# Optimization experiments

Hardware: AMD Instinct MI355X
Metric: run time of the kernel (lower is better)

## Reference

```python
import jax, jax.numpy as jnp
import numpy as np
from jax import lax

B, V, K, E = 32768, 256, 4, 2048
INTERVENTION_STRENGTH = 1.0
PROP_SCALE = 0.1
N_ROUNDS = 3


def setup_inputs() -> dict:
    key = jax.random.key(0)
    ks = jax.random.split(key, 20)
    s = 0.02
    return {
        "original_data": jax.random.normal(ks[0], (B, V), jnp.float32),
        "intervention_values": jax.random.normal(ks[1], (B, K), jnp.float32),
        "strengths": jax.random.uniform(ks[2], (E,), jnp.float32),
        "intervention_variables": jnp.arange(K, dtype=jnp.int32),
        "cause_idx": jax.random.randint(ks[3], (E,), 0, V, jnp.int32),
        "effect_idx": jax.random.randint(ks[4], (E,), 0, V, jnp.int32),
        # per-intervention-variable estimator MLPs: Linear(V,64) -> ReLU -> Linear(64,V)
        "est_W1": jax.random.normal(ks[5], (K, 64, V), jnp.float32) * s,
        "est_b1": jnp.zeros((K, 64), jnp.float32),
        "est_W2": jax.random.normal(ks[6], (K, V, 64), jnp.float32) * s,
        "est_b2": jnp.zeros((K, V), jnp.float32),
        # plausibility scorer: Linear(3V,128) -> ReLU -> Linear(128,64) -> ReLU -> Linear(64,1) -> Sigmoid
        "pl_W1": jax.random.normal(ks[7], (128, 3 * V), jnp.float32) * s,
        "pl_b1": jnp.zeros((128,), jnp.float32),
        "pl_W2": jax.random.normal(ks[8], (64, 128), jnp.float32) * s,
        "pl_b2": jnp.zeros((64,), jnp.float32),
        "pl_W3": jax.random.normal(ks[9], (1, 64), jnp.float32) * s,
        "pl_b3": jnp.zeros((1,), jnp.float32),
    }


def _propagate(data, cause_idx, effect_idx, strengths):
    # Faithful sequential in-place edge updates (effect of edge k may feed edge k+1).
    def step(d, ces):
        c, e, st = ces
        infl = d[:, c] * (st * PROP_SCALE)  # [B]
        return d.at[:, e].add(infl), None

    def round_body(d, _):
        d, _ = lax.scan(step, d, (cause_idx, effect_idx, strengths))
        return d, None

    d, _ = lax.scan(round_body, data, None, length=N_ROUNDS)
    return d


def reference(original_data, intervention_values, strengths,
              est_W1, est_b1, est_W2, est_b2,
              pl_W1, pl_b1, pl_W2, pl_b2, pl_W3, pl_b3,
              intervention_variables, cause_idx, effect_idx):
    x = original_data  # [B, V]
    ivars = intervention_variables  # [K] int, constant

    # do-intervention: overwrite selected columns
    intervened = x.at[:, ivars].set(intervention_values)  # [B, V]

    # intervention effect estimators, vectorized over the K intervened variables
    h = jax.nn.relu(jnp.einsum('bv,kov->bko', x, est_W1) + est_b1)          # [B, K, 64]
    eff = jnp.einsum('bko,kvo->bkv', h, est_W2) + est_b2                     # [B, K, V]
    mag = jnp.abs(intervention_values - x[:, ivars])                         # [B, K]
    intervention_effects = jnp.einsum('bkv,bk->bv', eff, mag) * INTERVENTION_STRENGTH  # [B, V]

    # sequential causal propagation over edge list, 3 rounds
    final_cf = _propagate(intervened + intervention_effects, cause_idx, effect_idx, strengths)

    # plausibility scorer MLP
    pin = jnp.concatenate([x, intervened, final_cf], axis=1)                 # [B, 3V]
    p = jax.nn.relu(pin @ pl_W1.T + pl_b1)
    p = jax.nn.relu(p @ pl_W2.T + pl_b2)
    plaus = jax.nn.sigmoid(p @ pl_W3.T + pl_b3)                              # [B, 1]

    impact = jnp.linalg.norm(final_cf - x, axis=1, keepdims=True)            # [B, 1]
    return final_cf, intervention_effects, plaus, impact
```

## Files before the change

kernel.cpp:

```cpp
#include <hip/hip_runtime.h>

#define BDIM 32768
#define VDIM 256
#define KVAR 4
#define EDIM 2048
#define SEGS 16
#define SEGLEN 128

typedef __attribute__((ext_vector_type(8))) short short8;
typedef __attribute__((ext_vector_type(4))) float f32x4;

__device__ __forceinline__ unsigned short f2b(float f){
  union { float f; unsigned u; } v; v.f = f;
  unsigned r = v.u + 0x7FFFu + ((v.u >> 16) & 1u);
  return (unsigned short)(r >> 16);
}
__device__ __forceinline__ float b2f(unsigned short h){
  union { unsigned u; float f; } v; v.u = ((unsigned)h) << 16;
  return v.f;
}
__device__ __forceinline__ short8 ldb8(const unsigned short* p){
  return *(const short8*)p;
}

__device__ __forceinline__ void gl_lds16(const unsigned short* g, unsigned short* l){
  __builtin_amdgcn_global_load_lds(
      (const __attribute__((address_space(1))) unsigned int*)g,
      (__attribute__((address_space(3))) unsigned int*)l, 16, 0, 0);
}

__device__ __forceinline__ void stage256(const unsigned short* Bt, int kB,
                                         int w, int lane, unsigned short* Bs){
#pragma unroll
  for (int i = 0; i < 4; i++){
    int g8 = i*8 + w;
    int r  = g8*8 + (lane >> 3);
    int s  = lane & 7;
    gl_lds16(Bt + (size_t)r*VDIM + kB + ((s ^ (r & 7)) << 3),
             Bs + (size_t)g8*512);
  }
}
__device__ __forceinline__ void stage128(const unsigned short* Bt, int kB,
                                         int w, int lane, unsigned short* Bs){
#pragma unroll
  for (int i = 0; i < 2; i++){
    int g8 = i*8 + w;
    int r  = g8*8 + (lane >> 3);
    int s  = lane & 7;
    gl_lds16(Bt + (size_t)r*VDIM + kB + ((s ^ (r & 7)) << 3),
             Bs + (size_t)g8*512);
  }
}

__device__ __forceinline__ short8 bs_frag(const unsigned short* Bs, int c, int klocal){
  int slot = klocal >> 3;
  return *(const short8*)&Bs[(size_t)c*64 + (((slot ^ (c & 7))) << 3)];
}

template<int NF>
__device__ __forceinline__ void mm_rA(const short8 (&a)[2][2], const unsigned short* Bs,
                                      int c0, int kb, f32x4 (&acc)[2][NF])
{
#pragma unroll
  for (int k = 0; k < 2; k++){
#pragma unroll
    for (int fn = 0; fn < NF; fn++){
      int c = c0 + fn*16;
      short8 b = bs_frag(Bs, c, k*32 + kb);
      acc[0][fn] = __builtin_amdgcn_mfma_f32_16x16x32_bf16(a[k][0], b, acc[0][fn], 0, 0, 0);
      acc[1][fn] = __builtin_amdgcn_mfma_f32_16x16x32_bf16(a[k][1], b, acc[1][fn], 0, 0, 0);
    }
  }
}
template<int NF>
__device__ __forceinline__ void mm_lA(const unsigned short* Alds, int ldaE,
                                      const unsigned short* Bs,
                                      int rl0, int c0, int kb, int kB,
                                      f32x4 (&acc)[2][NF])
{
  int sw = (rl0 & 7) << 3;
#pragma unroll
  for (int k = 0; k < 2; k++){
    int ka = kB + k*32 + kb;
    short8 a0 = *(const short8*)&Alds[(size_t)rl0 * ldaE + (ka ^ sw)];
    short8 a1 = *(const short8*)&Alds[(size_t)(rl0+16) * ldaE + (ka ^ sw)];
#pragma unroll
    for (int fn = 0; fn < NF; fn++){
      int c = c0 + fn*16;
      short8 b = bs_frag(Bs, c, k*32 + kb);
      acc[0][fn] = __builtin_amdgcn_mfma_f32_16x16x32_bf16(a0, b, acc[0][fn], 0, 0, 0);
      acc[1][fn] = __builtin_amdgcn_mfma_f32_16x16x32_bf16(a1, b, acc[1][fn], 0, 0, 0);
    }
  }
}
template<int NF, int KSZ>
__device__ __forceinline__ void mm_l1(const unsigned short* Alds, int ldaE,
                                      const unsigned short* Bt, int ldb,
                                      int rl0, int c0, int kb,
                                      f32x4 (&acc)[NF])
{
  int sw = (rl0 & 7) << 3;
#pragma unroll
  for (int k0 = 0; k0 < KSZ; k0 += 32){
    int ka = k0 + kb;
    short8 a0 = *(const short8*)&Alds[(size_t)rl0 * ldaE + (ka ^ sw)];
#pragma unroll
    for (int fn = 0; fn < NF; fn++){
      short8 b = ldb8(Bt + (size_t)(c0 + fn*16)*ldb + ka);
      acc[fn] = __builtin_amdgcn_mfma_f32_16x16x32_bf16(a0, b, acc[fn], 0, 0, 0);
    }
  }
}

__global__ __launch_bounds__(256) void prep_seg(
    const float* X, const float* IV, const int* ivars,
    const float* eW1, const float* eW2, const float* pW1, const float* pW2,
    const int* cidx, const int* eidx, const float* stren,
    unsigned short* XB,
    unsigned short* bt1, unsigned short* bt2,
    unsigned short* w1ab, unsigned short* w1c,
    unsigned short* w2bf, float* w1bcol, int* colmap,
    float* delta, float* segs)
{
  if (blockIdx.x < 1024){
    __shared__ int lc[SEGLEN];
    __shared__ int le[SEGLEN];
    __shared__ float la[SEGLEN];
    int bid = blockIdx.x;
    int seg = bid >> 6;
    int rowbase = (bid & 63) * 4;
    int w = threadIdx.x >> 6, lane = threadIdx.x & 63;
    int row = rowbase + w;
    int k0 = seg * SEGLEN;
    for (int t = threadIdx.x; t < SEGLEN; t += 256){
      lc[t] = cidx[k0 + t]; le[t] = eidx[k0 + t]; la[t] = stren[k0 + t] * 0.1f;
    }
    __syncthreads();
    float r0 = (row == lane)        ? 1.f : 0.f;
    float r1 = (row == lane + 64)   ? 1.f : 0.f;
    float r2 = (row == lane + 128)  ? 1.f : 0.f;
    float r3 = (row == lane + 192)  ? 1.f : 0.f;
    for (int t = 0; t < SEGLEN; t++){
      int cs = __builtin_amdgcn_readfirstlane(lc[t]);
      int es = __builtin_amdgcn_readfirstlane(le[t]);
      float a = la[t];
      float vr;
      switch (cs >> 6){ case 0: vr = r0; break; case 1: vr = r1; break;
                        case 2: vr = r2; break; default: vr = r3; }
      float v = __shfl(vr, cs & 63, 64);
      float add = (lane == (es & 63)) ? a * v : 0.f;
      switch (es >> 6){ case 0: r0 += add; break; case 1: r1 += add; break;
                        case 2: r2 += add; break; default: r3 += add; }
    }
    float* out = segs + (size_t)seg * 65536 + (size_t)row * 256;
    out[lane] = r0; out[lane + 64] = r1; out[lane + 128] = r2; out[lane + 192] = r3;
    return;
  }
  int stride = 1024 * 256;
  int g0 = (blockIdx.x - 1024) * 256 + threadIdx.x;
  for (int i = g0; i < (BDIM * VDIM) / 8; i += stride){
    const float* p = X + (size_t)i * 8;
    f32x4 lo = *(const f32x4*)p;
    f32x4 hi = *(const f32x4*)(p + 4);
    short8 r;
    r[0]=(short)f2b(lo[0]); r[1]=(short)f2b(lo[1]); r[2]=(short)f2b(lo[2]); r[3]=(short)f2b(lo[3]);
    r[4]=(short)f2b(hi[0]); r[5]=(short)f2b(hi[1]); r[6]=(short)f2b(hi[2]); r[7]=(short)f2b(hi[3]);
    *(short8*)(XB + (size_t)i * 8) = r;
  }
  for (int i = g0; i < 65536; i += stride) bt1[i] = f2b(eW1[i]);
  for (int i = g0; i < 65536; i += stride){
    int v = i >> 8, r = i & 255;
    bt2[i] = f2b(eW2[(r >> 6) * 16384 + v * 64 + (r & 63)]);
  }
  for (int i = g0; i < 32768; i += stride){
    int o = i >> 8, v = i & 255;
    w1ab[i] = f2b(pW1[o*768 + v] + pW1[o*768 + 256 + v]);
    w1c[i]  = f2b(pW1[o*768 + 512 + v]);
  }
  for (int i = g0; i < 8192; i += stride) w2bf[i] = f2b(pW2[i]);
  for (int i = g0; i < 512; i += stride){
    int o = i >> 2, k = i & 3;
    w1bcol[i] = pW1[o*768 + 256 + ivars[k]];
  }
  for (int i = g0; i < VDIM; i += stride){
    int m = -1;
#pragma unroll
    for (int k = 0; k < KVAR; k++) if (ivars[k] == i) m = k;
    colmap[i] = m;
  }
  for (int i = g0; i < BDIM * KVAR; i += stride){
    int b = i >> 2, k = i & 3;
    delta[i] = IV[i] - X[(size_t)b * VDIM + ivars[k]];
  }
}

__global__ __launch_bounds__(256) void combine4(const float* S, float* Out)
{
  int m = blockIdx.x >> 6;
  int rb = (blockIdx.x & 63) * 4;
  int c = threadIdx.x;
  __shared__ float v[4][256];
  const float* base = S + (size_t)m * 4 * 65536;
#pragma unroll
  for (int r = 0; r < 4; r++) v[r][c] = base[(size_t)(rb + r) * 256 + c];
  __syncthreads();
  for (int p = 1; p < 4; p++){
    const float* Bm = base + (size_t)p * 65536;
    float a0 = 0.f, a1 = 0.f, a2 = 0.f, a3 = 0.f;
    for (int k = 0; k < 256; k += 4){
      f32x4 v0 = *(const f32x4*)&v[0][k];
      f32x4 v1 = *(const f32x4*)&v[1][k];
      f32x4 v2 = *(const f32x4*)&v[2][k];
      f32x4 v3 = *(const f32x4*)&v[3][k];
#pragma unroll
      for (int j = 0; j < 4; j++){
        float bk = Bm[(size_t)(k + j) * 256 + c];
        a0 += v0[j] * bk; a1 += v1[j] * bk; a2 += v2[j] * bk; a3 += v3[j] * bk;
      }
    }
    __syncthreads();
    v[0][c] = a0; v[1][c] = a1; v[2][c] = a2; v[3][c] = a3;
    __syncthreads();
  }
#pragma unroll
  for (int r = 0; r < 4; r++) Out[(size_t)m * 65536 + (size_t)(rb + r) * 256 + c] = v[r][c];
}

__global__ __launch_bounds__(256) void powM(const float* R, unsigned short* Mt)
{
  int rb = blockIdx.x * 4;
  int c = threadIdx.x;
  __shared__ float v[4][256];
#pragma unroll
  for (int r = 0; r < 4; r++) v[r][c] = R[(size_t)(rb + r) * 256 + c];
  __syncthreads();
  for (int p = 0; p < 2; p++){
    float a0 = 0.f, a1 = 0.f, a2 = 0.f, a3 = 0.f;
    for (int k = 0; k < 256; k += 4){
      f32x4 v0 = *(const f32x4*)&v[0][k];
      f32x4 v1 = *(const f32x4*)&v[1][k];
      f32x4 v2 = *(const f32x4*)&v[2][k];
      f32x4 v3 = *(const f32x4*)&v[3][k];
#pragma unroll
      for (int j = 0; j < 4; j++){
        float bk = R[(size_t)(k + j) * 256 + c];
        a0 += v0[j] * bk; a1 += v1[j] * bk; a2 += v2[j] * bk; a3 += v3[j] * bk;
      }
    }
    __syncthreads();
    v[0][c] = a0; v[1][c] = a1; v[2][c] = a2; v[3][c] = a3;
    __syncthreads();
  }
#pragma unroll
  for (int r = 0; r < 4; r++) Mt[(size_t)c * 256 + (rb + r)] = f2b(v[r][c]);
}

__global__ __launch_bounds__(512, 4) void mega(
    const float* IV, const unsigned short* XB,
    const unsigned short* Bt1, const unsigned short* Bt2, const unsigned short* Mt,
    const unsigned short* W1ab, const unsigned short* W1c, const unsigned short* W2bf,
    const float* eb1, const float* eb2, const float* delta, const int* colmap,
    const float* w1bcol, const float* pb1, const float* pb2,
    const float* W3, const float* pb3,
    float* effOut, float* outF, float* plausOut, float* impOut)
{
  __shared__ unsigned short buf[64 * 256];
  __shared__ unsigned short Bs[256 * 64];
  __shared__ float impLds[64 * 4];
  int tid = threadIdx.x, w = tid >> 6, lane = tid & 63;
  int rowg = w >> 2, colg = w & 3;
  int rowBlk = blockIdx.x * 64;
  int rl0 = rowg * 32 + (lane & 15);
  int r0 = rowBlk + rl0;
  int colBase = colg * 64;
  int c0 = colBase + (lane & 15);
  int kb = (lane >> 4) * 8;
  f32x4 acc[2][4];

#pragma unroll
  for (int fm = 0; fm < 2; fm++)
#pragma unroll
    for (int fn = 0; fn < 4; fn++) acc[fm][fn] = (f32x4){0.f,0.f,0.f,0.f};
  for (int kc = 0; kc < 4; kc++){
    int kB = kc * 64;
    stage256(Bt1, kB, w, lane, Bs);
    short8 a[2][2];
#pragma unroll
    for (int k = 0; k < 2; k++)
#pragma unroll
      for (int m = 0; m < 2; m++)
        a[k][m] = ldb8(XB + (size_t)(r0 + m*16)*VDIM + kB + k*32 + kb);
    __syncthreads();
    __builtin_amdgcn_s_setprio(1);
    mm_rA<4>(a, Bs, c0, kb, acc);
    __builtin_amdgcn_s_setprio(0);
    __syncthreads();
  }
  {
    float b1v[4];
#pragma unroll
    for (int fn = 0; fn < 4; fn++) b1v[fn] = eb1[colBase + fn*16 + (lane & 15)];
#pragma unroll
    for (int fm = 0; fm < 2; fm++)
#pragma unroll
      for (int i = 0; i < 4; i++){
        int rl = rowg*32 + fm*16 + (lane >> 4)*4 + i;
        int gr = rowBlk + rl;
        float mg = fabsf(delta[gr*4 + colg]);
        int sw = (rl & 7) << 3;
#pragma unroll
        for (int fn = 0; fn < 4; fn++){
          int col = colBase + fn*16 + (lane & 15);
          float h = acc[fm][fn][i] + b1v[fn];
          h = h > 0.f ? h : 0.f;
          buf[(size_t)rl*256 + (col ^ sw)] = f2b(h * mg);
        }
      }
  }
  __syncthreads();

#pragma unroll
  for (int fm = 0; fm < 2; fm++)
#pragma unroll
    for (int fn = 0; fn < 4; fn++) acc[fm][fn] = (f32x4){0.f,0.f,0.f,0.f};
  for (int kc = 0; kc < 4; kc++){
    int kB = kc * 64;
    stage256(Bt2, kB, w, lane, Bs);
    __syncthreads();
    __builtin_amdgcn_s_setprio(1);
    mm_lA<4>(buf, 256, Bs, rl0, c0, kb, kB, acc);
    __builtin_amdgcn_s_setprio(0);
    __syncthreads();
  }
  {
    float bb0[4], bb1[4], bb2[4], bb3[4];
    int imv[4];
#pragma unroll
    for (int fn = 0; fn < 4; fn++){
      int col = colBase + fn*16 + (lane & 15);
      bb0[fn] = eb2[col]; bb1[fn] = eb2[256 + col];
      bb2[fn] = eb2[512 + col]; bb3[fn] = eb2[768 + col];
      imv[fn] = colmap[col];
    }
#pragma unroll
    for (int fm = 0; fm < 2; fm++)
#pragma unroll
      for (int i = 0; i < 4; i++){
        int rl = rowg*32 + fm*16 + (lane >> 4)*4 + i;
        int gr = rowBlk + rl;
        f32x4 dl = *(const f32x4*)&delta[gr*4];
        float d0a = fabsf(dl[0]), d1a = fabsf(dl[1]), d2a = fabsf(dl[2]), d3a = fabsf(dl[3]);
        int sw = (rl & 7) << 3;
#pragma unroll
        for (int fn = 0; fn < 4; fn++){
          int col = colBase + fn*16 + (lane & 15);
          float eff = acc[fm][fn][i] + d0a*bb0[fn] + d1a*bb1[fn] + d2a*bb2[fn] + d3a*bb3[fn];
          size_t idx = (size_t)gr*VDIM + col;
          __builtin_nontemporal_store(eff, &effOut[idx]);
          float base = (imv[fn] >= 0) ? IV[gr*4 + imv[fn]] : b2f(XB[idx]);
          buf[(size_t)rl*256 + (col ^ sw)] = f2b(base + eff);
        }
      }
  }
  __syncthreads();

#pragma unroll
  for (int fm = 0; fm < 2; fm++)
#pragma unroll
    for (int fn = 0; fn < 4; fn++) acc[fm][fn] = (f32x4){0.f,0.f,0.f,0.f};
  for (int kc = 0; kc < 4; kc++){
    int kB = kc * 64;
    stage256(Mt, kB, w, lane, Bs);
    __syncthreads();
    __builtin_amdgcn_s_setprio(1);
    mm_lA<4>(buf, 256, Bs, rl0, c0, kb, kB, acc);
    __builtin_amdgcn_s_setprio(0);
    __syncthreads();
  }
  {
#pragma unroll
    for (int fm = 0; fm < 2; fm++)
#pragma unroll
      for (int i = 0; i < 4; i++){
        int rl = rowg*32 + fm*16 + (lane >> 4)*4 + i;
        int gr = rowBlk + rl;
        int sw = (rl & 7) << 3;
        float ss = 0.f;
#pragma unroll
        for (int fn = 0; fn < 4; fn++){
          int col = colBase + fn*16 + (lane & 15);
          size_t idx = (size_t)gr*VDIM + col;
          float fv = acc[fm][fn][i];
          __builtin_nontemporal_store(fv, &outF[idx]);
          buf[(size_t)rl*256 + (col ^ sw)] = f2b(fv);
          float d = fv - b2f(XB[idx]);
          ss += d * d;
        }
        ss += __shfl_xor(ss, 1, 64); ss += __shfl_xor(ss, 2, 64);
        ss += __shfl_xor(ss, 4, 64); ss += __shfl_xor(ss, 8, 64);
        if ((lane & 15) == 0) impLds[rl*4 + colg] = ss;
      }
  }
  __syncthreads();

  {
    f32x4 a4[2][2];
#pragma unroll
    for (int fm = 0; fm < 2; fm++)
#pragma unroll
      for (int fn = 0; fn < 2; fn++) a4[fm][fn] = (f32x4){0.f,0.f,0.f,0.f};
    int c4 = colg * 32 + (lane & 15);
    for (int kc = 0; kc < 4; kc++){
      int kB = kc * 64;
      stage128(W1ab, kB, w, lane, Bs);
      stage128(W1c,  kB, w, lane, Bs + 8192);
      short8 a[2][2];
#pragma unroll
      for (int k = 0; k < 2; k++)
#pragma unroll
        for (int m = 0; m < 2; m++)
          a[k][m] = ldb8(XB + (size_t)(r0 + m*16)*VDIM + kB + k*32 + kb);
      __syncthreads();
      __builtin_amdgcn_s_setprio(1);
      mm_rA<2>(a, Bs, c4, kb, a4);
      mm_lA<2>(buf, 256, Bs + 8192, rl0, c4, kb, kB, a4);
      __builtin_amdgcn_s_setprio(0);
      __syncthreads();
    }
    float bv[2];
    f32x4 wb[2];
#pragma unroll
    for (int fn = 0; fn < 2; fn++){
      int col = colg*32 + fn*16 + (lane & 15);
      bv[fn] = pb1[col];
      wb[fn] = *(const f32x4*)&w1bcol[col*4];
    }
#pragma unroll
    for (int fm = 0; fm < 2; fm++)
#pragma unroll
      for (int i = 0; i < 4; i++){
        int rl = rowg*32 + fm*16 + (lane >> 4)*4 + i;
        int gr = rowBlk + rl;
        f32x4 dl = *(const f32x4*)&delta[gr*4];
        int sw = (rl & 7) << 3;
#pragma unroll
        for (int fn = 0; fn < 2; fn++){
          int col = colg*32 + fn*16 + (lane & 15);
          float p = a4[fm][fn][i] + bv[fn]
                  + dl[0]*wb[fn][0] + dl[1]*wb[fn][1] + dl[2]*wb[fn][2] + dl[3]*wb[fn][3];
          p = p > 0.f ? p : 0.f;
          buf[(size_t)rl*128 + (col ^ sw)] = f2b(p);
        }
      }
  }
  __syncthreads();

  if (w < 4){
    int rl0b = w * 16 + (lane & 15);
    f32x4 a2[4];
#pragma unroll
    for (int fn = 0; fn < 4; fn++) a2[fn] = (f32x4){0.f,0.f,0.f,0.f};
    mm_l1<4, 128>(buf, 128, W2bf, 128, rl0b, (lane & 15), kb, a2);
    float b2v[4], w3v[4];
#pragma unroll
    for (int fn = 0; fn < 4; fn++){
      int col = fn*16 + (lane & 15);
      b2v[fn] = pb2[col]; w3v[fn] = W3[col];
    }
    float b3v = pb3[0];
#pragma unroll
    for (int i = 0; i < 4; i++){
      float s = 0.f;
#pragma unroll
      for (int fn = 0; fn < 4; fn++){
        float p2 = a2[fn][i] + b2v[fn];
        p2 = p2 > 0.f ? p2 : 0.f;
        s += p2 * w3v[fn];
      }
      s += __shfl_xor(s, 1, 64); s += __shfl_xor(s, 2, 64);
      s += __shfl_xor(s, 4, 64); s += __shfl_xor(s, 8, 64);
      if ((lane & 15) == 0){
        int gr = rowBlk + w*16 + (lane >> 4)*4 + i;
        plausOut[gr] = 1.f / (1.f + expf(-(s + b3v)));
      }
    }
  } else if (w == 4){
    f32x4 v = *(const f32x4*)&impLds[lane * 4];
    impOut[rowBlk + lane] = sqrtf(v[0] + v[1] + v[2] + v[3]);
  }
}

#define WS_XB     ((size_t)0)
#define WS_DELTA  ((size_t)16777216)
#define WS_SEG    ((size_t)17301504)
#define WS_T2     ((size_t)21495808)
#define WS_R      ((size_t)22544384)
#define WS_MT     ((size_t)22806528)
#define WS_BT1    ((size_t)22937600)
#define WS_BT2    ((size_t)23068672)
#define WS_W1AB   ((size_t)23199744)
#define WS_W1C    ((size_t)23265280)
#define WS_W2BF   ((size_t)23330816)
#define WS_W1BCOL ((size_t)23347200)
#define WS_COLMAP ((size_t)23349248)

extern "C" void kernel_launch(void* const* d_in, const int* in_sizes, int n_in,
                              void* d_out, int out_size, void* d_ws, size_t ws_size,
                              hipStream_t stream)
{
  const float* X     = (const float*)d_in[0];
  const float* IV    = (const float*)d_in[1];
  const float* STR   = (const float*)d_in[2];
  const int*   IVARS = (const int*)d_in[3];
  const int*   CIDX  = (const int*)d_in[4];
  const int*   EIDX  = (const int*)d_in[5];
  const float* EW1   = (const float*)d_in[6];
  const float* EB1   = (const float*)d_in[7];
  const float* EW2   = (const float*)d_in[8];
  const float* EB2   = (const float*)d_in[9];
  const float* PW1   = (const float*)d_in[10];
  const float* PB1   = (const float*)d_in[11];
  const float* PW2   = (const float*)d_in[12];
  const float* PB2   = (const float*)d_in[13];
  const float* PW3   = (const float*)d_in[14];
  const float* PB3   = (const float*)d_in[15];

  char* ws = (char*)d_ws;
  unsigned short* XB     = (unsigned short*)(ws + WS_XB);
  float*          DELTA  = (float*)(ws + WS_DELTA);
  float*          SEG    = (float*)(ws + WS_SEG);
  float*          T2     = (float*)(ws + WS_T2);
  float*          Rm     = (float*)(ws + WS_R);
  unsigned short* MT     = (unsigned short*)(ws + WS_MT);
  unsigned short* BT1    = (unsigned short*)(ws + WS_BT1);
  unsigned short* BT2    = (unsigned short*)(ws + WS_BT2);
  unsigned short* W1AB   = (unsigned short*)(ws + WS_W1AB);
  unsigned short* W1C    = (unsigned short*)(ws + WS_W1C);
  unsigned short* W2BF   = (unsigned short*)(ws + WS_W2BF);
  float*          W1BCOL = (float*)(ws + WS_W1BCOL);
  int*            COLMAP = (int*)(ws + WS_COLMAP);

  float* outF   = (float*)d_out;
  float* outEff = outF + (size_t)BDIM * VDIM;
  float* outPl  = outEff + (size_t)BDIM * VDIM;
  float* outIm  = outPl + BDIM;

  prep_seg<<<2048, 256, 0, stream>>>(X, IV, IVARS, EW1, EW2, PW1, PW2,
                                     CIDX, EIDX, STR,
                                     XB, BT1, BT2, W1AB, W1C, W2BF, W1BCOL, COLMAP,
                                     DELTA, SEG);
  combine4<<<256, 256, 0, stream>>>(SEG, T2);
  combine4<<<64, 256, 0, stream>>>(T2, Rm);
  powM<<<64, 256, 0, stream>>>(Rm, MT);

  mega<<<512, 512, 0, stream>>>(IV, XB, BT1, BT2, MT, W1AB, W1C, W2BF,
                                EB1, EB2, DELTA, COLMAP, W1BCOL,
                                PB1, PB2, PW3, PB3,
                                outEff, outF, outPl, outIm);

  (void)in_sizes; (void)n_in; (void)out_size; (void)ws_size;
}
```

Baseline: 205.3 us.

## Double-buffer weight staging across all GEMM phases and cache X tile in LDS

The mega kernel now keeps two LDS weight buffers and prefetches the next weight chunk (across all four GEMM stages as one unit sequence) while the current chunk is multiplied. This removes one barrier per k-step and hides global-to-LDS latency. The block's 64x256 bf16 X tile is loaded once into LDS and reused for the first GEMM, the residual base, the impact norm and the scorer, replacing repeated global reads. Nontemporal stores become plain stores. LDS use roughly doubles to about 128KB, which drops the occupancy hint and may limit blocks per CU.

New measurement: 167.6 us (median of 2 runs). -18.4%, faster.

```diff
diff --git a/kernel.cpp b/kernel.cpp
--- a/kernel.cpp
+++ b/kernel.cpp
@@ -51,29 +51,25 @@
              Bs + (size_t)g8*512);
   }
 }
+__device__ __forceinline__ void stageA64(const unsigned short* XBg, int rowBlk,
+                                         int w, int lane, unsigned short* As){
+#pragma unroll
+  for (int i = 0; i < 4; i++){
+    int pair = i*8 + w;
+    int r = pair*2 + (lane >> 5);
+    int s = lane & 31;
+    gl_lds16(XBg + (size_t)(rowBlk + r)*VDIM + ((s ^ (r & 7)) << 3),
+             As + (size_t)pair*512);
+  }
+}
 
 __device__ __forceinline__ short8 bs_frag(const unsigned short* Bs, int c, int klocal){
   int slot = klocal >> 3;
-  return *(const short8*)&Bs[(size_t)c*64 + (((slot ^ (c & 7))) << 3)];
+  return *(const short8*)&Bs[(size_t)c*64 + ((slot ^ (c & 7)) << 3)];
 }
 
 template<int NF>
-__device__ __forceinline__ void mm_rA(const short8 (&a)[2][2], const unsigned short* Bs,
-                                      int c0, int kb, f32x4 (&acc)[2][NF])
-{
-#pragma unroll
-  for (int k = 0; k < 2; k++){
-#pragma unroll
-    for (int fn = 0; fn < NF; fn++){
-      int c = c0 + fn*16;
-      short8 b = bs_frag(Bs, c, k*32 + kb);
-      acc[0][fn] = __builtin_amdgcn_mfma_f32_16x16x32_bf16(a[k][0], b, acc[0][fn], 0, 0, 0);
-      acc[1][fn] = __builtin_amdgcn_mfma_f32_16x16x32_bf16(a[k][1], b, acc[1][fn], 0, 0, 0);
-    }
-  }
-}
-template<int NF>
-__device__ __forceinline__ void mm_lA(const unsigned short* Alds, int ldaE,
+__device__ __forceinline__ void mm_lA(const unsigned short* Alds,
                                       const unsigned short* Bs,
                                       int rl0, int c0, int kb, int kB,
                                       f32x4 (&acc)[2][NF])
@@ -82,12 +78,11 @@
 #pragma unroll
   for (int k = 0; k < 2; k++){
     int ka = kB + k*32 + kb;
-    short8 a0 = *(const short8*)&Alds[(size_t)rl0 * ldaE + (ka ^ sw)];
-    short8 a1 = *(const short8*)&Alds[(size_t)(rl0+16) * ldaE + (ka ^ sw)];
+    short8 a0 = *(const short8*)&Alds[(size_t)rl0 * 256 + (ka ^ sw)];
+    short8 a1 = *(const short8*)&Alds[(size_t)(rl0+16) * 256 + (ka ^ sw)];
 #pragma unroll
     for (int fn = 0; fn < NF; fn++){
-      int c = c0 + fn*16;
-      short8 b = bs_frag(Bs, c, k*32 + kb);
+      short8 b = bs_frag(Bs, c0 + fn*16, k*32 + kb);
       acc[0][fn] = __builtin_amdgcn_mfma_f32_16x16x32_bf16(a0, b, acc[0][fn], 0, 0, 0);
       acc[1][fn] = __builtin_amdgcn_mfma_f32_16x16x32_bf16(a1, b, acc[1][fn], 0, 0, 0);
     }
@@ -255,7 +250,7 @@
   for (int r = 0; r < 4; r++) Mt[(size_t)c * 256 + (rb + r)] = f2b(v[r][c]);
 }
 
-__global__ __launch_bounds__(512, 4) void mega(
+__global__ __launch_bounds__(512) void mega3(
     const float* IV, const unsigned short* XB,
     const unsigned short* Bt1, const unsigned short* Bt2, const unsigned short* Mt,
     const unsigned short* W1ab, const unsigned short* W1c, const unsigned short* W2bf,
@@ -264,35 +259,42 @@
     const float* W3, const float* pb3,
     float* effOut, float* outF, float* plausOut, float* impOut)
 {
+  __shared__ unsigned short xbs[64 * 256];
   __shared__ unsigned short buf[64 * 256];
-  __shared__ unsigned short Bs[256 * 64];
+  __shared__ unsigned short Bs0[256 * 64];
+  __shared__ unsigned short Bs1[256 * 64];
   __shared__ float impLds[64 * 4];
   int tid = threadIdx.x, w = tid >> 6, lane = tid & 63;
   int rowg = w >> 2, colg = w & 3;
   int rowBlk = blockIdx.x * 64;
   int rl0 = rowg * 32 + (lane & 15);
-  int r0 = rowBlk + rl0;
   int colBase = colg * 64;
   int c0 = colBase + (lane & 15);
   int kb = (lane >> 4) * 8;
   f32x4 acc[2][4];
 
+  auto stage_unit = [&](int u, unsigned short* Bs){
+    if (u < 4)       stage256(Bt1, u*64, w, lane, Bs);
+    else if (u < 8)  stage256(Bt2, (u-4)*64, w, lane, Bs);
+    else if (u < 12) stage256(Mt, (u-8)*64, w, lane, Bs);
+    else           { stage128(W1ab, (u-12)*64, w, lane, Bs);
+                     stage128(W1c,  (u-12)*64, w, lane, Bs + 8192); }
+  };
+
+  stageA64(XB, rowBlk, w, lane, xbs);
+  stage_unit(0, Bs0);
+  __syncthreads();
+
 #pragma unroll
   for (int fm = 0; fm < 2; fm++)
 #pragma unroll
     for (int fn = 0; fn < 4; fn++) acc[fm][fn] = (f32x4){0.f,0.f,0.f,0.f};
+#pragma unroll
   for (int kc = 0; kc < 4; kc++){
-    int kB = kc * 64;
-    stage256(Bt1, kB, w, lane, Bs);
-    short8 a[2][2];
-#pragma unroll
-    for (int k = 0; k < 2; k++)
-#pragma unroll
-      for (int m = 0; m < 2; m++)
-        a[k][m] = ldb8(XB + (size_t)(r0 + m*16)*VDIM + kB + k*32 + kb);
-    __syncthreads();
+    int u = kc;
+    stage_unit(u + 1, (u & 1) ? Bs0 : Bs1);
     __builtin_amdgcn_s_setprio(1);
-    mm_rA<4>(a, Bs, c0, kb, acc);
+    mm_lA<4>(xbs, (u & 1) ? Bs1 : Bs0, rl0, c0, kb, kc*64, acc);
     __builtin_amdgcn_s_setprio(0);
     __syncthreads();
   }
@@ -323,12 +325,12 @@
   for (int fm = 0; fm < 2; fm++)
 #pragma unroll
     for (int fn = 0; fn < 4; fn++) acc[fm][fn] = (f32x4){0.f,0.f,0.f,0.f};
+#pragma unroll
   for (int kc = 0; kc < 4; kc++){
-    int kB = kc * 64;
-    stage256(Bt2, kB, w, lane, Bs);
-    __syncthreads();
+    int u = 4 + kc;
+    stage_unit(u + 1, (u & 1) ? Bs0 : Bs1);
     __builtin_amdgcn_s_setprio(1);
-    mm_lA<4>(buf, 256, Bs, rl0, c0, kb, kB, acc);
+    mm_lA<4>(buf, (u & 1) ? Bs1 : Bs0, rl0, c0, kb, kc*64, acc);
     __builtin_amdgcn_s_setprio(0);
     __syncthreads();
   }
@@ -356,8 +358,9 @@
           int col = colBase + fn*16 + (lane & 15);
           float eff = acc[fm][fn][i] + d0a*bb0[fn] + d1a*bb1[fn] + d2a*bb2[fn] + d3a*bb3[fn];
           size_t idx = (size_t)gr*VDIM + col;
-          __builtin_nontemporal_store(eff, &effOut[idx]);
-          float base = (imv[fn] >= 0) ? IV[gr*4 + imv[fn]] : b2f(XB[idx]);
+          effOut[idx] = eff;
+          float base = (imv[fn] >= 0) ? IV[gr*4 + imv[fn]]
+                                      : b2f(xbs[(size_t)rl*256 + (col ^ sw)]);
           buf[(size_t)rl*256 + (col ^ sw)] = f2b(base + eff);
         }
       }
@@ -368,12 +371,12 @@
   for (int fm = 0; fm < 2; fm++)
 #pragma unroll
     for (int fn = 0; fn < 4; fn++) acc[fm][fn] = (f32x4){0.f,0.f,0.f,0.f};
+#pragma unroll
   for (int kc = 0; kc < 4; kc++){
-    int kB = kc * 64;
-    stage256(Mt, kB, w, lane, Bs);
-    __syncthreads();
+    int u = 8 + kc;
+    stage_unit(u + 1, (u & 1) ? Bs0 : Bs1);
     __builtin_amdgcn_s_setprio(1);
-    mm_lA<4>(buf, 256, Bs, rl0, c0, kb, kB, acc);
+    mm_lA<4>(buf, (u & 1) ? Bs1 : Bs0, rl0, c0, kb, kc*64, acc);
     __builtin_amdgcn_s_setprio(0);
     __syncthreads();
   }
@@ -391,9 +394,9 @@
           int col = colBase + fn*16 + (lane & 15);
           size_t idx = (size_t)gr*VDIM + col;
           float fv = acc[fm][fn][i];
-          __builtin_nontemporal_store(fv, &outF[idx]);
+          outF[idx] = fv;
           buf[(size_t)rl*256 + (col ^ sw)] = f2b(fv);
-          float d = fv - b2f(XB[idx]);
+          float d = fv - b2f(xbs[(size_t)rl*256 + (col ^ sw)]);
           ss += d * d;
         }
         ss += __shfl_xor(ss, 1, 64); ss += __shfl_xor(ss, 2, 64);
@@ -410,20 +413,14 @@
 #pragma unroll
       for (int fn = 0; fn < 2; fn++) a4[fm][fn] = (f32x4){0.f,0.f,0.f,0.f};
     int c4 = colg * 32 + (lane & 15);
+#pragma unroll
     for (int kc = 0; kc < 4; kc++){
-      int kB = kc * 64;
-      stage128(W1ab, kB, w, lane, Bs);
-      stage128(W1c,  kB, w, lane, Bs + 8192);
-      short8 a[2][2];
-#pragma unroll
-      for (int k = 0; k < 2; k++)
-#pragma unroll
-        for (int m = 0; m < 2; m++)
-          a[k][m] = ldb8(XB + (size_t)(r0 + m*16)*VDIM + kB + k*32 + kb);
-      __syncthreads();
+      int u = 12 + kc;
+      if (kc < 3) stage_unit(u + 1, (u & 1) ? Bs0 : Bs1);
+      const unsigned short* B = (u & 1) ? Bs1 : Bs0;
       __builtin_amdgcn_s_setprio(1);
-      mm_rA<2>(a, Bs, c4, kb, a4);
-      mm_lA<2>(buf, 256, Bs + 8192, rl0, c4, kb, kB, a4);
+      mm_lA<2>(xbs, B, rl0, c4, kb, kc*64, a4);
+      mm_lA<2>(buf, B + 8192, rl0, c4, kb, kc*64, a4);
       __builtin_amdgcn_s_setprio(0);
       __syncthreads();
     }
@@ -553,10 +550,10 @@
   combine4<<<64, 256, 0, stream>>>(T2, Rm);
   powM<<<64, 256, 0, stream>>>(Rm, MT);
 
-  mega<<<512, 512, 0, stream>>>(IV, XB, BT1, BT2, MT, W1AB, W1C, W2BF,
-                                EB1, EB2, DELTA, COLMAP, W1BCOL,
-                                PB1, PB2, PW3, PB3,
-                                outEff, outF, outPl, outIm);
+  mega3<<<512, 512, 0, stream>>>(IV, XB, BT1, BT2, MT, W1AB, W1C, W2BF,
+                                 EB1, EB2, DELTA, COLMAP, W1BCOL,
+                                 PB1, PB2, PW3, PB3,
+                                 outEff, outF, outPl, outIm);
 
   (void)in_sizes; (void)n_in; (void)out_size; (void)ws_size;
 }
```
